# Kernel tuning notes

Measured on AMD Instinct MI355X. Metric: run time of the kernel, lower is better.

## Reference

```python
import jax, jax.numpy as jnp
import numpy as np

B, S, D, H, F, E, K = 2, 2048, 1024, 16, 4096, 8, 2


def setup_inputs() -> dict:
    key = jax.random.key(0)
    ks = jax.random.split(key, 10)
    s = 0.02
    return {
        "x": jax.random.normal(ks[0], (B, S, D), jnp.float32),
        "ln_g": jnp.ones((D,), jnp.float32),
        "ln_b": jnp.zeros((D,), jnp.float32),
        "Wq": s * jax.random.normal(ks[1], (D, D), jnp.float32),
        "Wk": s * jax.random.normal(ks[2], (D, D), jnp.float32),
        "Wv": s * jax.random.normal(ks[3], (D, D), jnp.float32),
        "Wo": s * jax.random.normal(ks[4], (D, D), jnp.float32),
        "Wg": s * jax.random.normal(ks[5], (D, E), jnp.float32),
        "W1": s * jax.random.normal(ks[6], (E, D, F), jnp.float32),
        "b1": jnp.zeros((E, F), jnp.float32),
        "W2": s * jax.random.normal(ks[7], (E, F, D), jnp.float32),
        "b2": jnp.zeros((E, D), jnp.float32),
    }


def _layernorm(x, g, b, eps=1e-5):
    m = x.mean(-1, keepdims=True)
    v = x.var(-1, keepdims=True)
    return (x - m) * jax.lax.rsqrt(v + eps) * g + b


def reference(x, ln_g, ln_b, Wq, Wk, Wv, Wo, Wg, W1, b1, W2, b2):
    Bb, Ss, Dd = x.shape
    dh = Dd // H
    # --- pre-norm multi-head self-attention with residual ---
    h = _layernorm(x, ln_g, ln_b)
    q = (h @ Wq).reshape(Bb, Ss, H, dh)
    k = (h @ Wk).reshape(Bb, Ss, H, dh)
    v = (h @ Wv).reshape(Bb, Ss, H, dh)
    scores = jnp.einsum("bqhd,bkhd->bhqk", q, k) / np.sqrt(dh).astype(np.float32)
    attn = jax.nn.softmax(scores, axis=-1)
    o = jnp.einsum("bhqk,bkhd->bqhd", attn, v).reshape(Bb, Ss, Dd) @ Wo
    x = x + o
    # --- top-2 MoE with residual ---
    nE = Wg.shape[-1]
    probs = jax.nn.softmax(x @ Wg, axis=-1)  # [B,S,E]
    topv, topi = jax.lax.top_k(probs, K)
    topv = topv / topv.sum(-1, keepdims=True)
    w = (jax.nn.one_hot(topi, nE, dtype=x.dtype) * topv[..., None]).sum(-2)  # [B,S,E]
    h1 = jax.nn.gelu(jnp.einsum("bsd,edf->besf", x, W1) + b1[None, :, None, :])
    h2 = jnp.einsum("besf,efd->besd", h1, W2) + b2[None, :, None, :]
    out = x + jnp.einsum("bse,besd->bsd", w, h2)
    return out
```

## Files before the change

### kernel.cpp

```cpp
#include <hip/hip_runtime.h>
#include <hip/hip_bf16.h>

constexpr int Sc = 2048;
constexpr int Dc = 1024;
constexpr int Fc = 4096;
constexpr int Ec = 8;
constexpr int NTOK = 4096;

typedef __attribute__((ext_vector_type(8))) short short8;
typedef __attribute__((ext_vector_type(4))) float floatx4;
typedef unsigned short u16;

__device__ __forceinline__ u16 f2bf(float f) {
    __hip_bfloat16 h = __float2bfloat16(f);
    return *reinterpret_cast<u16*>(&h);
}

__device__ __forceinline__ float gelu_fast(float x) {
    float x2 = x * x;
    float z = x * fmaf(-0.07135481282f, x2, -1.5957691216057308f);
    float e = __expf(z);
    return x * __builtin_amdgcn_rcpf(1.0f + e);
}

__device__ __forceinline__ void async16(const u16* g, u16* l) {
    __builtin_amdgcn_global_load_lds(
        (const __attribute__((address_space(1))) unsigned int*)g,
        (__attribute__((address_space(3))) unsigned int*)l, 16, 0, 0);
}

__global__ __launch_bounds__(256) void tcast_kernel(const float* __restrict__ src,
                                                    u16* __restrict__ dst,
                                                    int R, int C,
                                                    size_t sstride, size_t dstride) {
    __shared__ float t[64][65];
    const float* s = src + (size_t)blockIdx.z * sstride;
    u16* d = dst + (size_t)blockIdx.z * dstride;
    int r0 = blockIdx.y * 64, c0 = blockIdx.x * 64;
    int tid = threadIdx.x;
#pragma unroll
    for (int i = 0; i < 4; i++) {
        int c = tid + i * 256;
        int row = c >> 4, col4 = (c & 15) * 4;
        float4 v = *(const float4*)(s + (size_t)(r0 + row) * C + c0 + col4);
        t[row][col4 + 0] = v.x;
        t[row][col4 + 1] = v.y;
        t[row][col4 + 2] = v.z;
        t[row][col4 + 3] = v.w;
    }
    __syncthreads();
#pragma unroll
    for (int i = 0; i < 2; i++) {
        int c = tid + i * 256;
        int dr = c >> 3, m8 = (c & 7) * 8;
        union { u16 us[8]; uint4 v; } pk;
#pragma unroll
        for (int j = 0; j < 8; j++) pk.us[j] = f2bf(t[m8 + j][dr]);
        *(uint4*)(d + (size_t)(c0 + dr) * R + r0 + m8) = pk.v;
    }
}

__global__ __launch_bounds__(256) void btrans_kernel(const u16* __restrict__ src,
                                                     u16* __restrict__ dst,
                                                     int R, int C) {
    __shared__ u16 t[64][72];
    int r0 = blockIdx.y * 64, c0 = blockIdx.x * 64;
    int tid = threadIdx.x;
#pragma unroll
    for (int i = 0; i < 2; i++) {
        int c = tid + i * 256;
        int row = c >> 3, s8 = (c & 7) * 8;
        *(uint4*)&t[row][s8] = *(const uint4*)(src + (size_t)(r0 + row) * C + c0 + s8);
    }
    __syncthreads();
#pragma unroll
    for (int i = 0; i < 2; i++) {
        int c = tid + i * 256;
        int row = c >> 3, s8 = (c & 7) * 8;
        union { u16 us[8]; uint4 v; } pk;
#pragma unroll
        for (int j = 0; j < 8; j++) pk.us[j] = t[s8 + j][row];
        *(uint4*)(dst + (size_t)(c0 + row) * R + r0 + s8) = pk.v;
    }
}

__global__ __launch_bounds__(256) void ln_kernel(const float* __restrict__ x,
                                                 const float* __restrict__ g,
                                                 const float* __restrict__ b,
                                                 u16* __restrict__ hb) {
    int row = blockIdx.x, tid = threadIdx.x;
    const float* xr = x + (size_t)row * Dc;
    float4 xv = ((const float4*)xr)[tid];
    float s = xv.x + xv.y + xv.z + xv.w;
    float ss = xv.x * xv.x + xv.y * xv.y + xv.z * xv.z + xv.w * xv.w;
    __shared__ float r1[256], r2[256];
    r1[tid] = s; r2[tid] = ss;
    __syncthreads();
    for (int off = 128; off > 0; off >>= 1) {
        if (tid < off) { r1[tid] += r1[tid + off]; r2[tid] += r2[tid + off]; }
        __syncthreads();
    }
    float mean = r1[0] * (1.0f / Dc);
    float var = r2[0] * (1.0f / Dc) - mean * mean;
    float rs = rsqrtf(var + 1e-5f);
    float4 gv = ((const float4*)g)[tid];
    float4 bv = ((const float4*)b)[tid];
    ushort4 o;
    o.x = f2bf((xv.x - mean) * rs * gv.x + bv.x);
    o.y = f2bf((xv.y - mean) * rs * gv.y + bv.y);
    o.z = f2bf((xv.z - mean) * rs * gv.z + bv.z);
    o.w = f2bf((xv.w - mean) * rs * gv.w + bv.w);
    *(ushort4*)(hb + (size_t)row * Dc + tid * 4) = o;
}

template <int MODE>
__global__ __launch_bounds__(256) void gemm_mfma(
    const u16* __restrict__ A, const u16* __restrict__ BT,
    int N, int K,
    u16* __restrict__ out_q, u16* __restrict__ out_k, u16* __restrict__ out_v,
    const float* __restrict__ resid, float* __restrict__ out_f32,
    u16* __restrict__ out_bf, const float* __restrict__ bias,
    const int* __restrict__ counts, const int* __restrict__ offsets,
    const int* __restrict__ list_tok) {
    int e = 0, cnt = 0, off = 0;
    if (MODE >= 2) {
        e = blockIdx.z;
        cnt = counts[e];
        if ((int)blockIdx.y * 128 >= cnt) return;
        off = offsets[e];
    }
    const int tid = threadIdx.x;
    const int m0 = blockIdx.y * 128, n0 = blockIdx.x * 128;
    __shared__ u16 As[128][32];
    __shared__ u16 Bs[128][32];
    __shared__ int toksL[128];
    if (MODE == 2) {
        if (tid < 128) toksL[tid] = list_tok[off + min(m0 + tid, cnt - 1)];
        __syncthreads();
    }
    const u16* Bbase = BT + (MODE >= 2 ? (size_t)e * (size_t)N * K : 0);
    const int w = tid >> 6, lane = tid & 63;
    const int wm = (w >> 1) * 64, wn = (w & 1) * 64;
    const int lr = lane & 15, lq = lane >> 4;

    const int rA0 = w * 32 + (lane >> 2), rA1 = rA0 + 16;
    const int gsegu = (((lane & 3) ^ ((lane >> 3) & 3))) * 8;
    size_t ra0, ra1;
    if (MODE == 2) {
        ra0 = (size_t)toksL[rA0] * K;
        ra1 = (size_t)toksL[rA1] * K;
    } else if (MODE == 3) {
        ra0 = (size_t)(off + min(m0 + rA0, cnt - 1)) * K;
        ra1 = (size_t)(off + min(m0 + rA1, cnt - 1)) * K;
    } else {
        ra0 = (size_t)(m0 + rA0) * K;
        ra1 = (size_t)(m0 + rA1) * K;
    }
    const u16* gA0 = A + ra0 + gsegu;
    const u16* gA1 = A + ra1 + gsegu;
    const u16* gB0 = Bbase + (size_t)(n0 + rA0) * K + gsegu;
    const u16* gB1 = Bbase + (size_t)(n0 + rA1) * K + gsegu;
    u16* ldsA0 = &As[w * 32][0];
    u16* ldsA1 = &As[w * 32 + 16][0];
    u16* ldsB0 = &Bs[w * 32][0];
    u16* ldsB1 = &Bs[w * 32 + 16][0];

    const int fs = (lq ^ ((lr >> 1) & 3)) * 8;
    const u16* apt[4];
    const u16* bpt[4];
#pragma unroll
    for (int i = 0; i < 4; i++) {
        apt[i] = &As[wm + i * 16 + lr][fs];
        bpt[i] = &Bs[wn + i * 16 + lr][fs];
    }

    floatx4 acc[4][4];
#pragma unroll
    for (int i = 0; i < 4; i++)
#pragma unroll
        for (int j = 0; j < 4; j++) acc[i][j] = (floatx4){0.f, 0.f, 0.f, 0.f};

    for (int k0 = 0; k0 < K; k0 += 32) {
        async16(gA0 + k0, ldsA0);
        async16(gA1 + k0, ldsA1);
        async16(gB0 + k0, ldsB0);
        async16(gB1 + k0, ldsB1);
        __syncthreads();
        short8 af[4], bfr[4];
#pragma unroll
        for (int i = 0; i < 4; i++) af[i] = *(const short8*)apt[i];
#pragma unroll
        for (int j = 0; j < 4; j++) bfr[j] = *(const short8*)bpt[j];
#pragma unroll
        for (int i = 0; i < 4; i++)
#pragma unroll
            for (int j = 0; j < 4; j++)
                acc[i][j] = __builtin_amdgcn_mfma_f32_16x16x32_bf16(af[i], bfr[j], acc[i][j], 0, 0, 0);
        __syncthreads();
    }

    if (MODE == 0) {
        int mat = n0 >> 10;
        u16* dst = (mat == 0) ? out_q : (mat == 1 ? out_k : out_v);
#pragma unroll
        for (int i = 0; i < 4; i++)
#pragma unroll
            for (int j = 0; j < 4; j++) {
                int cc = (n0 + wn + j * 16 + lr) & 1023;
                int row0 = m0 + wm + i * 16 + lq * 4;
#pragma unroll
                for (int r = 0; r < 4; r++)
                    dst[(size_t)(row0 + r) * 1024 + cc] = f2bf(acc[i][j][r]);
            }
    } else if (MODE == 1) {
#pragma unroll
        for (int i = 0; i < 4; i++)
#pragma unroll
            for (int j = 0; j < 4; j++) {
                int col = n0 + wn + j * 16 + lr;
                int row0 = m0 + wm + i * 16 + lq * 4;
#pragma unroll
                for (int r = 0; r < 4; r++) {
                    size_t idx = (size_t)(row0 + r) * 1024 + col;
                    float v = acc[i][j][r] + resid[idx];
                    out_f32[idx] = v;
                    out_bf[idx] = f2bf(v);
                }
            }
    } else if (MODE == 2) {
#pragma unroll
        for (int j = 0; j < 4; j++) {
            int col = n0 + wn + j * 16 + lr;
            float bv = bias[(size_t)e * 4096 + col];
#pragma unroll
            for (int i = 0; i < 4; i++) {
                int rl0 = m0 + wm + i * 16 + lq * 4;
#pragma unroll
                for (int r = 0; r < 4; r++) {
                    if (rl0 + r < cnt)
                        out_bf[(size_t)(off + rl0 + r) * 4096 + col] = f2bf(gelu_fast(acc[i][j][r] + bv));
                }
            }
        }
    } else {
#pragma unroll
        for (int j = 0; j < 4; j++) {
            int col = n0 + wn + j * 16 + lr;
            float bv = bias[(size_t)e * 1024 + col];
#pragma unroll
            for (int i = 0; i < 4; i++) {
                int rl0 = m0 + wm + i * 16 + lq * 4;
#pragma unroll
                for (int r = 0; r < 4; r++) {
                    if (rl0 + r < cnt)
                        out_f32[(size_t)(off + rl0 + r) * 1024 + col] = acc[i][j][r] + bv;
                }
            }
        }
    }
}

__global__ __launch_bounds__(256) void attn_mfma(const u16* __restrict__ qb,
                                                 const u16* __restrict__ kb,
                                                 const u16* __restrict__ vt,
                                                 u16* __restrict__ aob) {
    __shared__ u16 qs[64][72], ks[64][72], vs[64][72], ps[64][72];
    const int q0 = blockIdx.x * 64, h = blockIdx.y, b = blockIdx.z;
    const int tid = threadIdx.x, w = tid >> 6, lane = tid & 63;
    const int lr = lane & 15, lq = lane >> 4;
    const int ms = w * 16;
    const size_t tok0 = (size_t)b * Sc;

#pragma unroll
    for (int i = 0; i < 2; i++) {
        int c = tid + i * 256;
        int row = c >> 3, d8 = (c & 7) * 8;
        *(uint4*)&qs[row][d8] = *(const uint4*)(qb + (tok0 + q0 + row) * 1024 + h * 64 + d8);
    }
    __syncthreads();
    short8 qa[2];
    qa[0] = *(const short8*)&qs[ms + lr][lq * 8];
    qa[1] = *(const short8*)&qs[ms + lr][32 + lq * 8];

    floatx4 oacc[4];
    float m_r[4], l_r[4];
#pragma unroll
    for (int d4 = 0; d4 < 4; d4++) oacc[d4] = (floatx4){0.f, 0.f, 0.f, 0.f};
#pragma unroll
    for (int r = 0; r < 4; r++) { m_r[r] = -1e30f; l_r[r] = 0.f; }

    for (int kt = 0; kt < Sc / 64; kt++) {
        int k0 = kt * 64;
        __syncthreads();
#pragma unroll
        for (int i = 0; i < 2; i++) {
            int c = tid + i * 256;
            int row = c >> 3, d8 = (c & 7) * 8;
            *(uint4*)&ks[row][d8] = *(const uint4*)(kb + (tok0 + k0 + row) * 1024 + h * 64 + d8);
            *(uint4*)&vs[row][d8] = *(const uint4*)(vt + (size_t)(h * 64 + row) * 4096 + tok0 + k0 + d8);
        }
        __syncthreads();
        floatx4 sfr[4];
#pragma unroll
        for (int j4 = 0; j4 < 4; j4++) {
            short8 kf0 = *(const short8*)&ks[j4 * 16 + lr][lq * 8];
            short8 kf1 = *(const short8*)&ks[j4 * 16 + lr][32 + lq * 8];
            floatx4 sa = (floatx4){0.f, 0.f, 0.f, 0.f};
            sa = __builtin_amdgcn_mfma_f32_16x16x32_bf16(qa[0], kf0, sa, 0, 0, 0);
            sa = __builtin_amdgcn_mfma_f32_16x16x32_bf16(qa[1], kf1, sa, 0, 0, 0);
            sfr[j4] = sa * 0.125f;
        }
#pragma unroll
        for (int r = 0; r < 4; r++) {
            float mx = fmaxf(fmaxf(sfr[0][r], sfr[1][r]), fmaxf(sfr[2][r], sfr[3][r]));
            mx = fmaxf(mx, __shfl_xor(mx, 1, 64));
            mx = fmaxf(mx, __shfl_xor(mx, 2, 64));
            mx = fmaxf(mx, __shfl_xor(mx, 4, 64));
            mx = fmaxf(mx, __shfl_xor(mx, 8, 64));
            float mn = fmaxf(m_r[r], mx);
            float alpha = __expf(m_r[r] - mn);
            m_r[r] = mn;
            float rs = 0.f;
#pragma unroll
            for (int j4 = 0; j4 < 4; j4++) {
                float p = __expf(sfr[j4][r] - mn);
                sfr[j4][r] = p;
                rs += p;
            }
            rs += __shfl_xor(rs, 1, 64);
            rs += __shfl_xor(rs, 2, 64);
            rs += __shfl_xor(rs, 4, 64);
            rs += __shfl_xor(rs, 8, 64);
            l_r[r] = l_r[r] * alpha + rs;
#pragma unroll
            for (int d4 = 0; d4 < 4; d4++) oacc[d4][r] *= alpha;
        }
#pragma unroll
        for (int j4 = 0; j4 < 4; j4++)
#pragma unroll
            for (int r = 0; r < 4; r++)
                ps[ms + lq * 4 + r][j4 * 16 + lr] = f2bf(sfr[j4][r]);
        __syncthreads();
        short8 pa0 = *(const short8*)&ps[ms + lr][lq * 8];
        short8 pa1 = *(const short8*)&ps[ms + lr][32 + lq * 8];
#pragma unroll
        for (int d4 = 0; d4 < 4; d4++) {
            short8 vf0 = *(const short8*)&vs[d4 * 16 + lr][lq * 8];
            short8 vf1 = *(const short8*)&vs[d4 * 16 + lr][32 + lq * 8];
            oacc[d4] = __builtin_amdgcn_mfma_f32_16x16x32_bf16(pa0, vf0, oacc[d4], 0, 0, 0);
            oacc[d4] = __builtin_amdgcn_mfma_f32_16x16x32_bf16(pa1, vf1, oacc[d4], 0, 0, 0);
        }
    }
#pragma unroll
    for (int r = 0; r < 4; r++) {
        float inv = 1.0f / l_r[r];
        size_t row = tok0 + q0 + ms + lq * 4 + r;
#pragma unroll
        for (int d4 = 0; d4 < 4; d4++)
            aob[row * 1024 + h * 64 + d4 * 16 + lr] = f2bf(oacc[d4][r] * inv);
    }
}

__global__ __launch_bounds__(256) void router_kernel(const float* __restrict__ x2,
                                                     const float* __restrict__ Wg,
                                                     int* __restrict__ topi,
                                                     float* __restrict__ topw,
                                                     int* __restrict__ counts) {
    int t = blockIdx.x, tid = threadIdx.x;
    float p[Ec] = {};
    const float* xr = x2 + (size_t)t * Dc;
    for (int k = tid; k < Dc; k += 256) {
        float xv = xr[k];
        const float* wr = Wg + (size_t)k * Ec;
#pragma unroll
        for (int e = 0; e < Ec; e++) p[e] += xv * wr[e];
    }
    __shared__ float red[256 * Ec];
#pragma unroll
    for (int e = 0; e < Ec; e++) red[tid * Ec + e] = p[e];
    __syncthreads();
    for (int off = 128; off > 0; off >>= 1) {
        if (tid < off) {
#pragma unroll
            for (int e = 0; e < Ec; e++) red[tid * Ec + e] += red[(tid + off) * Ec + e];
        }
        __syncthreads();
    }
    if (tid == 0) {
        float l[Ec];
        float mx = -1e30f;
#pragma unroll
        for (int e = 0; e < Ec; e++) { l[e] = red[e]; mx = fmaxf(mx, l[e]); }
#pragma unroll
        for (int e = 0; e < Ec; e++) l[e] = __expf(l[e] - mx);
        int i0 = 0;
#pragma unroll
        for (int e = 1; e < Ec; e++) if (l[e] > l[i0]) i0 = e;
        int i1 = (i0 == 0) ? 1 : 0;
#pragma unroll
        for (int e = 0; e < Ec; e++) if (e != i0 && l[e] > l[i1]) i1 = e;
        float v0 = l[i0], v1 = l[i1];
        float inv = 1.0f / (v0 + v1);
        topi[t * 2 + 0] = i0;
        topi[t * 2 + 1] = i1;
        topw[t * 2 + 0] = v0 * inv;
        topw[t * 2 + 1] = v1 * inv;
        atomicAdd(&counts[i0], 1);
        atomicAdd(&counts[i1], 1);
    }
}

__global__ void zero_small(int* counts, int* cursor) {
    int i = threadIdx.x;
    if (i < Ec) { counts[i] = 0; cursor[i] = 0; }
}

__global__ void scan_kernel(const int* counts, int* offsets) {
    if (threadIdx.x == 0) {
        int s = 0;
        for (int e = 0; e < Ec; e++) { offsets[e] = s; s += counts[e]; }
    }
}

__global__ __launch_bounds__(256) void scatter_kernel(const int* __restrict__ topi,
                                                      const int* __restrict__ offsets,
                                                      int* __restrict__ cursor,
                                                      int* __restrict__ list_tok,
                                                      int* __restrict__ slot_of) {
    int t = blockIdx.x * 256 + threadIdx.x;
    if (t >= NTOK) return;
    for (int s2 = 0; s2 < 2; s2++) {
        int e = topi[t * 2 + s2];
        int p = offsets[e] + atomicAdd(&cursor[e], 1);
        list_tok[p] = t;
        slot_of[t * 2 + s2] = p;
    }
}

__global__ __launch_bounds__(256) void combine_kernel(const float* __restrict__ x2,
                                                      const float* __restrict__ h2,
                                                      const int* __restrict__ slot_of,
                                                      const float* __restrict__ topw,
                                                      float* __restrict__ out) {
    int t = blockIdx.x, c = threadIdx.x;
    int s0 = slot_of[t * 2], s1 = slot_of[t * 2 + 1];
    float w0 = topw[t * 2], w1 = topw[t * 2 + 1];
    float4 a = ((const float4*)(x2 + (size_t)t * Dc))[c];
    float4 h0 = ((const float4*)(h2 + (size_t)s0 * Dc))[c];
    float4 h1 = ((const float4*)(h2 + (size_t)s1 * Dc))[c];
    float4 o;
    o.x = a.x + w0 * h0.x + w1 * h1.x;
    o.y = a.y + w0 * h0.y + w1 * h1.y;
    o.z = a.z + w0 * h0.z + w1 * h1.z;
    o.w = a.w + w0 * h0.w + w1 * h1.w;
    ((float4*)(out + (size_t)t * Dc))[c] = o;
}

extern "C" void kernel_launch(void* const* d_in, const int* in_sizes, int n_in,
                              void* d_out, int out_size, void* d_ws, size_t ws_size,
                              hipStream_t stream) {
    const float* x    = (const float*)d_in[0];
    const float* ln_g = (const float*)d_in[1];
    const float* ln_b = (const float*)d_in[2];
    const float* Wq   = (const float*)d_in[3];
    const float* Wk   = (const float*)d_in[4];
    const float* Wv   = (const float*)d_in[5];
    const float* Wo   = (const float*)d_in[6];
    const float* Wg   = (const float*)d_in[7];
    const float* W1   = (const float*)d_in[8];
    const float* b1   = (const float*)d_in[9];
    const float* W2   = (const float*)d_in[10];
    const float* b2   = (const float*)d_in[11];
    float* out = (float*)d_out;

    char* ws = (char*)d_ws;
    const size_t MB = 1ull << 20;
    float* x2    = (float*)(ws + 0 * MB);
    u16* x2b     = (u16*)(ws + 16 * MB);
    u16* hb      = (u16*)(ws + 24 * MB);
    u16* wqkvT   = (u16*)(ws + 32 * MB);
    u16* woT     = (u16*)(ws + 38 * MB);
    u16* qb      = (u16*)(ws + 40 * MB);
    u16* kb      = (u16*)(ws + 48 * MB);
    u16* vt      = (u16*)(ws + 56 * MB);
    u16* vb      = (u16*)(ws + 64 * MB);
    u16* aob     = (u16*)(ws + 64 * MB);
    u16* w1T     = (u16*)(ws + 72 * MB);
    u16* w2T     = (u16*)(ws + 136 * MB);
    u16* h1      = (u16*)(ws + 200 * MB);
    float* h2    = (float*)(ws + 264 * MB);
    char* sm     = ws + 296 * MB;
    float* topw    = (float*)(sm);
    int*   topi    = (int*)(sm + (1 << 15));
    int*   slot_of = (int*)(sm + 2 * (1 << 15));
    int*   list_tok= (int*)(sm + 3 * (1 << 15));
    int*   counts  = (int*)(sm + 4 * (1 << 15));
    int*   offsets = counts + 64;
    int*   cursor  = counts + 128;

    tcast_kernel<<<dim3(16, 16, 1), 256, 0, stream>>>(Wq, wqkvT + 0 * 1024 * 1024, 1024, 1024, 0, 0);
    tcast_kernel<<<dim3(16, 16, 1), 256, 0, stream>>>(Wk, wqkvT + 1 * 1024 * 1024, 1024, 1024, 0, 0);
    tcast_kernel<<<dim3(16, 16, 1), 256, 0, stream>>>(Wv, wqkvT + 2 * 1024 * 1024, 1024, 1024, 0, 0);
    tcast_kernel<<<dim3(16, 16, 1), 256, 0, stream>>>(Wo, woT, 1024, 1024, 0, 0);
    tcast_kernel<<<dim3(64, 16, 8), 256, 0, stream>>>(W1, w1T, 1024, 4096,
                                                      (size_t)1024 * 4096, (size_t)4096 * 1024);
    tcast_kernel<<<dim3(16, 64, 8), 256, 0, stream>>>(W2, w2T, 4096, 1024,
                                                      (size_t)4096 * 1024, (size_t)1024 * 4096);

    ln_kernel<<<NTOK, 256, 0, stream>>>(x, ln_g, ln_b, hb);
    gemm_mfma<0><<<dim3(24, 32), 256, 0, stream>>>(hb, wqkvT, 3072, 1024,
                                                   qb, kb, vb, nullptr, nullptr, nullptr, nullptr,
                                                   nullptr, nullptr, nullptr);
    btrans_kernel<<<dim3(16, 64), 256, 0, stream>>>(vb, vt, 4096, 1024);
    attn_mfma<<<dim3(Sc / 64, 16, 2), 256, 0, stream>>>(qb, kb, vt, aob);
    gemm_mfma<1><<<dim3(8, 32), 256, 0, stream>>>(aob, woT, 1024, 1024,
                                                  nullptr, nullptr, nullptr, x, x2, x2b, nullptr,
                                                  nullptr, nullptr, nullptr);

    zero_small<<<1, 64, 0, stream>>>(counts, cursor);
    router_kernel<<<NTOK, 256, 0, stream>>>(x2, Wg, topi, topw, counts);
    scan_kernel<<<1, 1, 0, stream>>>(counts, offsets);
    scatter_kernel<<<NTOK / 256, 256, 0, stream>>>(topi, offsets, cursor, list_tok, slot_of);

    gemm_mfma<2><<<dim3(32, 32, 8), 256, 0, stream>>>(x2b, w1T, 4096, 1024,
                                                      nullptr, nullptr, nullptr, nullptr, nullptr,
                                                      h1, b1, counts, offsets, list_tok);
    gemm_mfma<3><<<dim3(8, 32, 8), 256, 0, stream>>>(h1, w2T, 1024, 4096,
                                                     nullptr, nullptr, nullptr, nullptr, h2,
                                                     nullptr, b2, counts, offsets, list_tok);
    combine_kernel<<<NTOK, 256, 0, stream>>>(x2, h2, slot_of, topw, out);
}
```

Baseline: 979.9 us.

## Add 256x256 double-buffered GEMM with split-K for QKV and MoE expert GEMMs

Introduces a new 512-thread GEMM kernel with 256x256 tiles, 64-wide K steps, double-buffered LDS fed by async global-to-LDS loads, XOR swizzling, and interleaved barriers with MFMA priority hints. It is used for the QKV projection and both expert FFN GEMMs, and the second expert GEMM is split along K into two halves written to separate buffers that the combine kernel sums. The goal is more data reuse per tile and better overlap of loads with MFMA work. In exchange it adds partial-tile waste for uneven expert counts and an extra fp32 partial buffer that reuses the workspace region of the attention q buffer.

```diff
diff --git a/kernel.cpp b/kernel.cpp
--- a/kernel.cpp
+++ b/kernel.cpp
@@ -28,6 +28,8 @@
         (const __attribute__((address_space(1))) unsigned int*)g,
         (__attribute__((address_space(3))) unsigned int*)l, 16, 0, 0);
 }
+
+#define BAR() asm volatile("s_barrier" ::: "memory")
 
 __global__ __launch_bounds__(256) void tcast_kernel(const float* __restrict__ src,
                                                     u16* __restrict__ dst,
@@ -122,40 +124,19 @@
     u16* __restrict__ out_bf, const float* __restrict__ bias,
     const int* __restrict__ counts, const int* __restrict__ offsets,
     const int* __restrict__ list_tok) {
-    int e = 0, cnt = 0, off = 0;
-    if (MODE >= 2) {
-        e = blockIdx.z;
-        cnt = counts[e];
-        if ((int)blockIdx.y * 128 >= cnt) return;
-        off = offsets[e];
-    }
     const int tid = threadIdx.x;
     const int m0 = blockIdx.y * 128, n0 = blockIdx.x * 128;
     __shared__ u16 As[128][32];
     __shared__ u16 Bs[128][32];
-    __shared__ int toksL[128];
-    if (MODE == 2) {
-        if (tid < 128) toksL[tid] = list_tok[off + min(m0 + tid, cnt - 1)];
-        __syncthreads();
-    }
-    const u16* Bbase = BT + (MODE >= 2 ? (size_t)e * (size_t)N * K : 0);
+    const u16* Bbase = BT;
     const int w = tid >> 6, lane = tid & 63;
     const int wm = (w >> 1) * 64, wn = (w & 1) * 64;
     const int lr = lane & 15, lq = lane >> 4;
 
     const int rA0 = w * 32 + (lane >> 2), rA1 = rA0 + 16;
     const int gsegu = (((lane & 3) ^ ((lane >> 3) & 3))) * 8;
-    size_t ra0, ra1;
-    if (MODE == 2) {
-        ra0 = (size_t)toksL[rA0] * K;
-        ra1 = (size_t)toksL[rA1] * K;
-    } else if (MODE == 3) {
-        ra0 = (size_t)(off + min(m0 + rA0, cnt - 1)) * K;
-        ra1 = (size_t)(off + min(m0 + rA1, cnt - 1)) * K;
-    } else {
-        ra0 = (size_t)(m0 + rA0) * K;
-        ra1 = (size_t)(m0 + rA1) * K;
-    }
+    size_t ra0 = (size_t)(m0 + rA0) * K;
+    size_t ra1 = (size_t)(m0 + rA1) * K;
     const u16* gA0 = A + ra0 + gsegu;
     const u16* gA1 = A + ra1 + gsegu;
     const u16* gB0 = Bbase + (size_t)(n0 + rA0) * K + gsegu;
@@ -199,62 +180,200 @@
         __syncthreads();
     }
 
-    if (MODE == 0) {
-        int mat = n0 >> 10;
-        u16* dst = (mat == 0) ? out_q : (mat == 1 ? out_k : out_v);
-#pragma unroll
-        for (int i = 0; i < 4; i++)
-#pragma unroll
-            for (int j = 0; j < 4; j++) {
-                int cc = (n0 + wn + j * 16 + lr) & 1023;
-                int row0 = m0 + wm + i * 16 + lq * 4;
-#pragma unroll
-                for (int r = 0; r < 4; r++)
-                    dst[(size_t)(row0 + r) * 1024 + cc] = f2bf(acc[i][j][r]);
-            }
-    } else if (MODE == 1) {
-#pragma unroll
-        for (int i = 0; i < 4; i++)
-#pragma unroll
-            for (int j = 0; j < 4; j++) {
-                int col = n0 + wn + j * 16 + lr;
-                int row0 = m0 + wm + i * 16 + lq * 4;
-#pragma unroll
-                for (int r = 0; r < 4; r++) {
-                    size_t idx = (size_t)(row0 + r) * 1024 + col;
-                    float v = acc[i][j][r] + resid[idx];
-                    out_f32[idx] = v;
-                    out_bf[idx] = f2bf(v);
-                }
-            }
-    } else if (MODE == 2) {
+#pragma unroll
+    for (int i = 0; i < 4; i++)
 #pragma unroll
         for (int j = 0; j < 4; j++) {
             int col = n0 + wn + j * 16 + lr;
-            float bv = bias[(size_t)e * 4096 + col];
-#pragma unroll
-            for (int i = 0; i < 4; i++) {
-                int rl0 = m0 + wm + i * 16 + lq * 4;
-#pragma unroll
-                for (int r = 0; r < 4; r++) {
+            int row0 = m0 + wm + i * 16 + lq * 4;
+#pragma unroll
+            for (int r = 0; r < 4; r++) {
+                size_t idx = (size_t)(row0 + r) * 1024 + col;
+                float v = acc[i][j][r] + resid[idx];
+                out_f32[idx] = v;
+                out_bf[idx] = f2bf(v);
+            }
+        }
+}
+
+template <int MODE>
+__global__ __launch_bounds__(512, 2) void gemm256(
+    const u16* __restrict__ A, const u16* __restrict__ BT, int Nn, int Kfull,
+    u16* __restrict__ out_q, u16* __restrict__ out_k, u16* __restrict__ out_v,
+    u16* __restrict__ out_bf, float* __restrict__ o32a, float* __restrict__ o32b,
+    const float* __restrict__ bias,
+    const int* __restrict__ counts, const int* __restrict__ offsets,
+    const int* __restrict__ list_tok) {
+    __shared__ u16 smem[66048];
+    int e = 0, cnt = 0, off = 0, ks = 0;
+    if (MODE >= 2) {
+        e = (MODE == 3) ? ((int)blockIdx.z >> 1) : (int)blockIdx.z;
+        if (MODE == 3) ks = (int)blockIdx.z & 1;
+        cnt = counts[e];
+        if ((int)blockIdx.y * 256 >= cnt) return;
+        off = offsets[e];
+    }
+    const int tid = threadIdx.x;
+    const int m0 = blockIdx.y * 256, n0 = blockIdx.x * 256;
+    const int w = tid >> 6, lane = tid & 63;
+    const int wm = w >> 2, wn = w & 3;
+    const int lr = lane & 15, lq = lane >> 4;
+    const int sz8 = (lr & 7) << 3;
+
+    int* toksL = (int*)(smem + 65536);
+    if (MODE == 2) {
+        if (tid < 256) toksL[tid] = list_tok[off + min(m0 + tid, cnt - 1)];
+        __syncthreads();
+    }
+    const int K = Kfull;
+    const int NT = (MODE == 3 ? 2048 : K) / 64;
+    const size_t kb = (MODE == 3) ? (size_t)ks * 2048 : 0;
+    const u16* Bb = BT + (MODE >= 2 ? (size_t)e * (size_t)Nn * K : (size_t)0);
+
+    const u16* srcA[4];
+    const u16* srcB[4];
+    {
+        const int rl8 = w * 8 + (lane >> 3);
+        const int sg = ((lane & 7) ^ (lane >> 3)) * 8;
+#pragma unroll
+        for (int i = 0; i < 4; i++) {
+            int rA = i * 64 + rl8;
+            size_t gr;
+            if (MODE == 2) gr = (size_t)toksL[rA];
+            else if (MODE == 3) gr = (size_t)(off + min(m0 + rA, cnt - 1));
+            else gr = (size_t)(m0 + rA);
+            srcA[i] = A + gr * K + kb + sg;
+            srcB[i] = Bb + (size_t)(n0 + rA) * K + kb + sg;
+        }
+    }
+
+    short8 areg[4][2], breg[4][2];
+    floatx4 acc[8][4];
+#pragma unroll
+    for (int i = 0; i < 8; i++)
+#pragma unroll
+        for (int j = 0; j < 4; j++) acc[i][j] = (floatx4){0.f, 0.f, 0.f, 0.f};
+
+#define STG(kt, mat, h)                                                            \
+    do {                                                                           \
+        u16* _ld = smem + ((kt) & 1) * 32768 + (mat) * 16384 + (h) * 8192 + w * 512; \
+        async16(((mat) ? srcB : srcA)[(h) * 2 + 0] + (size_t)(kt) * 64, _ld);      \
+        async16(((mat) ? srcB : srcA)[(h) * 2 + 1] + (size_t)(kt) * 64, _ld + 4096); \
+    } while (0)
+
+    auto ldA = [&](int bufp, int mq) {
+        const u16* ah = smem + bufp * 32768 + wm * 8192 + (mq * 64 + lr) * 64;
+#pragma unroll
+        for (int mf = 0; mf < 4; mf++)
+#pragma unroll
+            for (int kk = 0; kk < 2; kk++)
+                areg[mf][kk] = *(const short8*)(ah + mf * 1024 + ((kk * 32 + lq * 8) ^ sz8));
+    };
+    const int bBo = 16384 + (wn >> 1) * 8192 + (wn & 1) * 4096 + lr * 64;
+    auto ldB01 = [&](int bufp) {
+        const u16* bh = smem + bufp * 32768 + bBo;
+#pragma unroll
+        for (int kk = 0; kk < 2; kk++) {
+            breg[0][kk] = *(const short8*)(bh + ((kk * 32 + lq * 8) ^ sz8));
+            breg[1][kk] = *(const short8*)(bh + 1024 + ((kk * 32 + lq * 8) ^ sz8));
+        }
+    };
+    auto ldB23 = [&](int bufp) {
+        const u16* bh = smem + bufp * 32768 + bBo;
+#pragma unroll
+        for (int kk = 0; kk < 2; kk++) {
+            breg[2][kk] = *(const short8*)(bh + 2048 + ((kk * 32 + lq * 8) ^ sz8));
+            breg[3][kk] = *(const short8*)(bh + 3072 + ((kk * 32 + lq * 8) ^ sz8));
+        }
+    };
+
+#define MMQ(MB, NB)                                                                  \
+    do {                                                                             \
+        __builtin_amdgcn_s_setprio(1);                                               \
+        _Pragma("unroll") for (int kk = 0; kk < 2; kk++) {                           \
+            _Pragma("unroll") for (int mi = 0; mi < 4; mi++) {                       \
+                acc[(MB) + mi][(NB) + 0] = __builtin_amdgcn_mfma_f32_16x16x32_bf16(  \
+                    areg[mi][kk], breg[(NB) + 0][kk], acc[(MB) + mi][(NB) + 0], 0, 0, 0); \
+                acc[(MB) + mi][(NB) + 1] = __builtin_amdgcn_mfma_f32_16x16x32_bf16(  \
+                    areg[mi][kk], breg[(NB) + 1][kk], acc[(MB) + mi][(NB) + 1], 0, 0, 0); \
+            }                                                                        \
+        }                                                                            \
+        __builtin_amdgcn_s_setprio(0);                                               \
+    } while (0)
+
+    STG(0, 1, 0); STG(0, 0, 0); STG(0, 0, 1); STG(0, 1, 1);
+    STG(1, 1, 0); STG(1, 0, 0);
+
+    for (int t = 0; t < NT; ++t) {
+        const int bp = t & 1;
+        if (t + 1 < NT) STG(t + 1, 0, 1);
+        if (t == NT - 1) { asm volatile("s_waitcnt vmcnt(0)" ::: "memory"); }
+        else             { asm volatile("s_waitcnt vmcnt(6)" ::: "memory"); }
+        BAR();
+        ldA(bp, 0);
+        ldB01(bp);
+        MMQ(0, 0);
+        BAR();
+        ldB23(bp);
+        if (t + 1 < NT) STG(t + 1, 1, 1);
+        BAR();
+        MMQ(0, 2);
+        BAR();
+        ldA(bp, 1);
+        if (t + 2 < NT) STG(t + 2, 1, 0);
+        BAR();
+        MMQ(4, 0);
+        BAR();
+        if (t + 2 < NT) STG(t + 2, 0, 0);
+        BAR();
+        MMQ(4, 2);
+        BAR();
+    }
+#undef STG
+#undef MMQ
+
+    if (MODE == 0) {
+        const int mat = n0 >> 10;
+        u16* dst = (mat == 0) ? out_q : (mat == 1 ? out_k : out_v);
+#pragma unroll
+        for (int fi = 0; fi < 8; fi++) {
+            const int row0 = m0 + wm * 128 + fi * 16 + lq * 4;
+#pragma unroll
+            for (int nj = 0; nj < 4; nj++) {
+                const int cc = (n0 + wn * 64 + nj * 16 + lr) & 1023;
+#pragma unroll
+                for (int r = 0; r < 4; r++)
+                    dst[(size_t)(row0 + r) * 1024 + cc] = f2bf(acc[fi][nj][r]);
+            }
+        }
+    } else if (MODE == 2) {
+#pragma unroll
+        for (int nj = 0; nj < 4; nj++) {
+            const int col = n0 + wn * 64 + nj * 16 + lr;
+            const float bv = bias[(size_t)e * 4096 + col];
+#pragma unroll
+            for (int fi = 0; fi < 8; fi++) {
+                const int rl0 = m0 + wm * 128 + fi * 16 + lq * 4;
+#pragma unroll
+                for (int r = 0; r < 4; r++)
                     if (rl0 + r < cnt)
-                        out_bf[(size_t)(off + rl0 + r) * 4096 + col] = f2bf(gelu_fast(acc[i][j][r] + bv));
-                }
+                        out_bf[(size_t)(off + rl0 + r) * 4096 + col] =
+                            f2bf(gelu_fast(acc[fi][nj][r] + bv));
             }
         }
-    } else {
-#pragma unroll
-        for (int j = 0; j < 4; j++) {
-            int col = n0 + wn + j * 16 + lr;
-            float bv = bias[(size_t)e * 1024 + col];
-#pragma unroll
-            for (int i = 0; i < 4; i++) {
-                int rl0 = m0 + wm + i * 16 + lq * 4;
-#pragma unroll
-                for (int r = 0; r < 4; r++) {
+    } else if (MODE == 3) {
+        float* o = ks ? o32b : o32a;
+#pragma unroll
+        for (int nj = 0; nj < 4; nj++) {
+            const int col = n0 + wn * 64 + nj * 16 + lr;
+            const float bv = ks ? 0.f : bias[(size_t)e * 1024 + col];
+#pragma unroll
+            for (int fi = 0; fi < 8; fi++) {
+                const int rl0 = m0 + wm * 128 + fi * 16 + lq * 4;
+#pragma unroll
+                for (int r = 0; r < 4; r++)
                     if (rl0 + r < cnt)
-                        out_f32[(size_t)(off + rl0 + r) * 1024 + col] = acc[i][j][r] + bv;
-                }
+                        o[(size_t)(off + rl0 + r) * 1024 + col] = acc[fi][nj][r] + bv;
             }
         }
     }
@@ -438,7 +557,8 @@
 }
 
 __global__ __launch_bounds__(256) void combine_kernel(const float* __restrict__ x2,
-                                                      const float* __restrict__ h2,
+                                                      const float* __restrict__ h2a,
+                                                      const float* __restrict__ h2b,
                                                       const int* __restrict__ slot_of,
                                                       const float* __restrict__ topw,
                                                       float* __restrict__ out) {
@@ -446,13 +566,15 @@
     int s0 = slot_of[t * 2], s1 = slot_of[t * 2 + 1];
     float w0 = topw[t * 2], w1 = topw[t * 2 + 1];
     float4 a = ((const float4*)(x2 + (size_t)t * Dc))[c];
-    float4 h0 = ((const float4*)(h2 + (size_t)s0 * Dc))[c];
-    float4 h1 = ((const float4*)(h2 + (size_t)s1 * Dc))[c];
+    float4 p0 = ((const float4*)(h2a + (size_t)s0 * Dc))[c];
+    float4 q0 = ((const float4*)(h2b + (size_t)s0 * Dc))[c];
+    float4 p1 = ((const float4*)(h2a + (size_t)s1 * Dc))[c];
+    float4 q1 = ((const float4*)(h2b + (size_t)s1 * Dc))[c];
     float4 o;
-    o.x = a.x + w0 * h0.x + w1 * h1.x;
-    o.y = a.y + w0 * h0.y + w1 * h1.y;
-    o.z = a.z + w0 * h0.z + w1 * h1.z;
-    o.w = a.w + w0 * h0.w + w1 * h1.w;
+    o.x = a.x + w0 * (p0.x + q0.x) + w1 * (p1.x + q1.x);
+    o.y = a.y + w0 * (p0.y + q0.y) + w1 * (p1.y + q1.y);
+    o.z = a.z + w0 * (p0.z + q0.z) + w1 * (p1.z + q1.z);
+    o.w = a.w + w0 * (p0.w + q0.w) + w1 * (p1.w + q1.w);
     ((float4*)(out + (size_t)t * Dc))[c] = o;
 }
 
@@ -485,6 +607,7 @@
     u16* vt      = (u16*)(ws + 56 * MB);
     u16* vb      = (u16*)(ws + 64 * MB);
     u16* aob     = (u16*)(ws + 64 * MB);
+    float* h2b   = (float*)(ws + 40 * MB);
     u16* w1T     = (u16*)(ws + 72 * MB);
     u16* w2T     = (u16*)(ws + 136 * MB);
     u16* h1      = (u16*)(ws + 200 * MB);
@@ -508,9 +631,9 @@
                                                       (size_t)4096 * 1024, (size_t)1024 * 4096);
 
     ln_kernel<<<NTOK, 256, 0, stream>>>(x, ln_g, ln_b, hb);
-    gemm_mfma<0><<<dim3(24, 32), 256, 0, stream>>>(hb, wqkvT, 3072, 1024,
-                                                   qb, kb, vb, nullptr, nullptr, nullptr, nullptr,
-                                                   nullptr, nullptr, nullptr);
+    gemm256<0><<<dim3(12, 16, 1), 512, 0, stream>>>(hb, wqkvT, 3072, 1024,
+                                                    qb, kb, vb, nullptr, nullptr, nullptr,
+                                                    nullptr, nullptr, nullptr, nullptr);
     btrans_kernel<<<dim3(16, 64), 256, 0, stream>>>(vb, vt, 4096, 1024);
     attn_mfma<<<dim3(Sc / 64, 16, 2), 256, 0, stream>>>(qb, kb, vt, aob);
     gemm_mfma<1><<<dim3(8, 32), 256, 0, stream>>>(aob, woT, 1024, 1024,
@@ -522,11 +645,13 @@
     scan_kernel<<<1, 1, 0, stream>>>(counts, offsets);
     scatter_kernel<<<NTOK / 256, 256, 0, stream>>>(topi, offsets, cursor, list_tok, slot_of);
 
-    gemm_mfma<2><<<dim3(32, 32, 8), 256, 0, stream>>>(x2b, w1T, 4096, 1024,
-                                                      nullptr, nullptr, nullptr, nullptr, nullptr,
-                                                      h1, b1, counts, offsets, list_tok);
-    gemm_mfma<3><<<dim3(8, 32, 8), 256, 0, stream>>>(h1, w2T, 1024, 4096,
-                                                     nullptr, nullptr, nullptr, nullptr, h2,
-                                                     nullptr, b2, counts, offsets, list_tok);
-    combine_kernel<<<NTOK, 256, 0, stream>>>(x2, h2, slot_of, topw, out);
-}
+    gemm256<2><<<dim3(16, 16, 8), 512, 0, stream>>>(x2b, w1T, 4096, 1024,
+                                                    nullptr, nullptr, nullptr,
+                                                    h1, nullptr, nullptr, b1,
+                                                    counts, offsets, list_tok);
+    gemm256<3><<<dim3(4, 16, 16), 512, 0, stream>>>(h1, w2T, 1024, 4096,
+                                                    nullptr, nullptr, nullptr,
+                                                    nullptr, h2, h2b, b2,
+                                                    counts, offsets, list_tok);
+    combine_kernel<<<NTOK, 256, 0, stream>>>(x2, h2, h2b, slot_of, topw, out);
+}
```

Result: no change. 974.9 us (-0.5%).
